# Kernel tuning notes

Hardware: AMD Instinct MI355X
Metric: run time of the kernel (lower is better)

## Reference

```python
import jax, jax.numpy as jnp
import numpy as np

N_NODES = 50000
N_EDGES = 800000
DIMS = [128, 512, 256, 128]
EPS = 1e-5


def setup_inputs() -> dict:
    key = jax.random.key(0)
    ks = jax.random.split(key, 2 + 5 * 3)
    inp = {
        "x": jax.random.normal(ks[0], (N_NODES, DIMS[0]), dtype=jnp.float32),
        "edge_index": jax.random.randint(ks[1], (2, N_EDGES), 0, N_NODES, dtype=jnp.int64),
    }
    ki = 2
    for i in range(3):
        din, dout = DIMS[i], DIMS[i + 1]
        s = 1.0 / np.sqrt(din)
        inp[f"Wl{i}"] = jax.random.uniform(ks[ki + 0], (din, dout), jnp.float32, -s, s)
        inp[f"bl{i}"] = jax.random.uniform(ks[ki + 1], (dout,), jnp.float32, -s, s)
        inp[f"Wr{i}"] = jax.random.uniform(ks[ki + 2], (din, dout), jnp.float32, -s, s)
        inp[f"g{i}"] = jnp.ones((dout,), jnp.float32)
        inp[f"b{i}"] = jnp.zeros((dout,), jnp.float32)
        ki += 5
    return inp


def _sage_mean(x, src, dst, Wl, bl, Wr):
    n = x.shape[0]
    agg = jax.ops.segment_sum(x[src], dst, num_segments=n)  # [N, din]
    deg = jax.ops.segment_sum(jnp.ones((src.shape[0],), x.dtype), dst, num_segments=n)
    mean = agg / jnp.maximum(deg, 1.0)[:, None]
    return mean @ Wl + bl + x @ Wr


def _bn(h, gamma, beta):
    m = h.mean(axis=0)
    v = h.var(axis=0)
    return gamma * (h - m) * jax.lax.rsqrt(v + EPS) + beta


def reference(x, edge_index, Wl0, bl0, Wr0, g0, b0, Wl1, bl1, Wr1, g1, b1, Wl2, bl2, Wr2, g2, b2):
    src, dst = edge_index[0], edge_index[1]
    params = [(Wl0, bl0, Wr0, g0, b0), (Wl1, bl1, Wr1, g1, b1), (Wl2, bl2, Wr2, g2, b2)]
    h = x
    for Wl, bl, Wr, g, b in params:
        h = _sage_mean(h, src, dst, Wl, bl, Wr)
        h = _bn(h, g, b)
        h = jax.nn.relu(h)
        # dropout: identity in eval mode
    return h
```

## Files before the change

kernel.cpp:

```cpp
#include <hip/hip_runtime.h>
#include <cstdint>
#include <cstddef>


#define EPS_BN 1e-5f

typedef unsigned short ushort_t;
typedef __attribute__((ext_vector_type(8))) short short8;
typedef __attribute__((ext_vector_type(4))) float float4v;
typedef __attribute__((ext_vector_type(2))) float float2v;
typedef __attribute__((ext_vector_type(2))) unsigned int uint2v;
typedef __attribute__((ext_vector_type(4))) unsigned int uint4v;

__device__ __forceinline__ float bflo(unsigned int w) {
    union { unsigned int i; float f; } v; v.i = w << 16; return v.f;
}
__device__ __forceinline__ float bfhi(unsigned int w) {
    union { unsigned int i; float f; } v; v.i = w & 0xffff0000u; return v.f;
}
__device__ __forceinline__ ushort_t f2bf(float f) {
    union { float f; unsigned int i; } v; v.f = f;
    unsigned int r = v.i + 0x7fffu + ((v.i >> 16) & 1u);
    return (ushort_t)(r >> 16);
}

__device__ __forceinline__ void async_copy16(void* lds, const void* g) {
    __builtin_amdgcn_global_load_lds(
        (const __attribute__((address_space(1))) unsigned int*)g,
        (__attribute__((address_space(3))) unsigned int*)lds, 16, 0, 0);
}

__device__ __forceinline__ void edge_sd(const int* __restrict__ p, int e, int ne,
                                        bool is64, int& s, int& d) {
    if (is64) { s = p[2 * e];  d = p[2 * ne + 2 * e]; }
    else      { s = p[e];      d = p[ne + e]; }
}
__device__ __forceinline__ int edge_d(const int* __restrict__ p, int e, int ne, bool is64) {
    return is64 ? p[2 * ne + 2 * e] : p[ne + e];
}

__device__ __forceinline__ bool detect_is64(const int* __restrict__ edges,
                                            int* sh_flag, int t) {
    if (t == 0) *sh_flag = 1;
    __syncthreads();
    if (t < 64 && edges[2 * t + 1] != 0) *sh_flag = 0;
    __syncthreads();
    return *sh_flag != 0;
}

#define EPB 2048

__global__ __launch_bounds__(256) void bhist_kernel(
    const int* __restrict__ edges, int ne, int* __restrict__ gcnt) {
    __shared__ int h[256];
    __shared__ int f64;
    int t = threadIdx.x;
    bool is64 = detect_is64(edges, &f64, t);
    h[t] = 0;
    __syncthreads();
    int base_e = blockIdx.x * EPB;
    #pragma unroll
    for (int u = 0; u < EPB / 256; ++u) {
        int i = base_e + u * 256 + t;
        if (i < ne) atomicAdd(&h[edge_d(edges, i, ne, is64) >> 8], 1);
    }
    __syncthreads();
    if (h[t]) atomicAdd(&gcnt[t], h[t]);
}

__global__ __launch_bounds__(256) void bscan_kernel(
    const int* __restrict__ gcnt, int nb, int ne,
    int* __restrict__ bbase, int* __restrict__ bcur) {
    __shared__ int sh[256];
    int t = threadIdx.x;
    int v = (t < nb) ? gcnt[t] : 0;
    sh[t] = v;
    __syncthreads();
    for (int o = 1; o < 256; o <<= 1) {
        int x = (t >= o) ? sh[t - o] : 0;
        __syncthreads();
        sh[t] += x;
        __syncthreads();
    }
    int excl = sh[t] - v;
    if (t < nb) { bbase[t] = excl; bcur[t] = excl; }
    if (t == nb) bbase[t] = ne;
    if (t == 0 && nb == 256) bbase[256] = ne;
}

__global__ __launch_bounds__(256) void bscatter_kernel(
    const int* __restrict__ edges, int ne,
    int* __restrict__ bcur, int* __restrict__ packed) {
    __shared__ int h[256];
    __shared__ int chunkb[256];
    __shared__ int lcur[256];
    __shared__ int f64;
    int t = threadIdx.x;
    bool is64 = detect_is64(edges, &f64, t);
    h[t] = 0;
    lcur[t] = 0;
    __syncthreads();
    int base_e = blockIdx.x * EPB;
    int ent[EPB / 256], eb[EPB / 256];
    #pragma unroll
    for (int u = 0; u < EPB / 256; ++u) {
        int i = base_e + u * 256 + t;
        if (i < ne) {
            int s, d;
            edge_sd(edges, i, ne, is64, s, d);
            ent[u] = s | ((d & 255) << 24);
            eb[u] = d >> 8;
            atomicAdd(&h[eb[u]], 1);
        } else eb[u] = -1;
    }
    __syncthreads();
    if (h[t]) chunkb[t] = atomicAdd(&bcur[t], h[t]);
    __syncthreads();
    #pragma unroll
    for (int u = 0; u < EPB / 256; ++u) {
        if (eb[u] >= 0) {
            int lp = atomicAdd(&lcur[eb[u]], 1);
            packed[chunkb[eb[u]] + lp] = ent[u];
        }
    }
}

__global__ __launch_bounds__(256) void bbuild_kernel(
    const int* __restrict__ packed, const int* __restrict__ bbase,
    int* __restrict__ rowptr, int* __restrict__ csr_src, int n) {
    __shared__ int h[256];
    __shared__ int cur[256];
    int t = threadIdx.x;
    int bb = blockIdx.x;
    int base = bbase[bb], cnt = bbase[bb + 1] - base;
    h[t] = 0;
    __syncthreads();
    for (int i = t; i < cnt; i += 256)
        atomicAdd(&h[(unsigned)packed[base + i] >> 24], 1);
    __syncthreads();
    int v = h[t];
    for (int o = 1; o < 256; o <<= 1) {
        int x = (t >= o) ? h[t - o] : 0;
        __syncthreads();
        h[t] += x;
        __syncthreads();
    }
    int excl = h[t] - v;
    int node = bb * 256 + t;
    if (node <= n) rowptr[node] = base + excl;
    cur[t] = excl;
    __syncthreads();
    for (int i = t; i < cnt; i += 256) {
        int e = packed[base + i];
        int lp = atomicAdd(&cur[(unsigned)e >> 24], 1);
        csr_src[base + lp] = e & 0xffffff;
    }
}

__global__ void prep_all_kernel(
    const float* __restrict__ x, ushort_t* __restrict__ xb, int nxb,
    const float* __restrict__ Wl0, const float* __restrict__ Wr0,
    ushort_t* __restrict__ WT0, int nb0,
    const float* __restrict__ Wl1, const float* __restrict__ Wr1,
    ushort_t* __restrict__ WT1c, int nb1,
    const float* __restrict__ Wl2, const float* __restrict__ Wr2,
    ushort_t* __restrict__ WT2c) {
    const int D0 = 128, D1 = 512, D2 = 256, D3 = 128;
    int b = blockIdx.x;
    if (b < nxb) {
        int i = b * 256 + threadIdx.x;
        xb[i] = f2bf(x[i]);
        return;
    }
    b -= nxb;
    if (b < nb0) {
        int idx = b * 256 + threadIdx.x;
        int K2 = 2 * D0;
        int nn = idx / K2, k = idx - nn * K2;
        float v = (k < D0) ? Wl0[(size_t)k * D1 + nn] : Wr0[(size_t)(k - D0) * D1 + nn];
        WT0[idx] = f2bf(v);
        return;
    }
    b -= nb0;
    if (b < nb1) {
        int idx = b * 256 + threadIdx.x;
        int nn = idx / D1, k = idx - nn * D1;
        float v = (nn < D2) ? Wl1[(size_t)k * D2 + nn] : Wr1[(size_t)k * D2 + (nn - D2)];
        WT1c[idx] = f2bf(v);
        return;
    }
    b -= nb1;
    {
        int idx = b * 256 + threadIdx.x;
        int nn = idx / D2, k = idx - nn * D2;
        float v = (nn < D3) ? Wl2[(size_t)k * D3 + nn] : Wr2[(size_t)k * D3 + (nn - D3)];
        WT2c[idx] = f2bf(v);
    }
}

template <int VEC> struct VecT;
template <> struct VecT<2> { using T = unsigned int; };
template <> struct VecT<4> { using T = uint2v; };
template <> struct VecT<8> { using T = uint4v; };

template <int VEC>
__device__ __forceinline__ void vunpack(typename VecT<VEC>::T v, unsigned int* w) {
    if constexpr (VEC == 2) { w[0] = v; }
    else if constexpr (VEC == 4) { w[0] = v.x; w[1] = v.y; }
    else { w[0] = v.x; w[1] = v.y; w[2] = v.z; w[3] = v.w; }
}

template <int VEC>
__device__ __forceinline__ void vaccum(typename VecT<VEC>::T v, float* acc) {
    unsigned int w[VEC / 2];
    vunpack<VEC>(v, w);
    #pragma unroll
    for (int i = 0; i < VEC / 2; ++i) {
        acc[2 * i + 0] += bflo(w[i]);
        acc[2 * i + 1] += bfhi(w[i]);
    }
}

template <int VEC>
__device__ __forceinline__ void gather_sum(
    const ushort_t* __restrict__ base, const int* __restrict__ csr_src,
    int e0, int e1, int rstride, float* acc) {
    using VT = typename VecT<VEC>::T;
    int e = e0;
    for (; e + 16 <= e1; e += 16) {
        VT v[16];
        #pragma unroll
        for (int u = 0; u < 16; ++u)
            v[u] = *(const VT*)(base + (size_t)csr_src[e + u] * rstride);
        #pragma unroll
        for (int u = 0; u < 16; ++u) vaccum<VEC>(v[u], acc);
    }
    if (e + 8 <= e1) {
        VT v[8];
        #pragma unroll
        for (int u = 0; u < 8; ++u)
            v[u] = *(const VT*)(base + (size_t)csr_src[e + u] * rstride);
        #pragma unroll
        for (int u = 0; u < 8; ++u) vaccum<VEC>(v[u], acc);
        e += 8;
    }
    if (e + 4 <= e1) {
        VT v[4];
        #pragma unroll
        for (int u = 0; u < 4; ++u)
            v[u] = *(const VT*)(base + (size_t)csr_src[e + u] * rstride);
        #pragma unroll
        for (int u = 0; u < 4; ++u) vaccum<VEC>(v[u], acc);
        e += 4;
    }
    if (e + 2 <= e1) {
        VT v0 = *(const VT*)(base + (size_t)csr_src[e] * rstride);
        VT v1 = *(const VT*)(base + (size_t)csr_src[e + 1] * rstride);
        vaccum<VEC>(v0, acc); vaccum<VEC>(v1, acc);
        e += 2;
    }
    if (e < e1)
        vaccum<VEC>(*(const VT*)(base + (size_t)csr_src[e] * rstride), acc);
}

template <int VEC>
__global__ __launch_bounds__(256) void aggregate_wave_kernel(
    const ushort_t* __restrict__ h, ushort_t* __restrict__ mean,
    const int* __restrict__ rowptr, const int* __restrict__ csr_src, int nnodes) {
    const int din = VEC * 64;
    const int wave = threadIdx.x >> 6;
    const int lane = threadIdx.x & 63;
    const int wstride = gridDim.x * 4;
    using VT = typename VecT<VEC>::T;
    for (int wid = blockIdx.x * 4 + wave; wid < nnodes; wid += wstride) {
        int e0 = rowptr[wid], e1 = rowptr[wid + 1];
        float acc[VEC];
        #pragma unroll
        for (int i = 0; i < VEC; ++i) acc[i] = 0.f;
        gather_sum<VEC>(h + (size_t)lane * VEC, csr_src, e0, e1, din, acc);

        int deg = e1 - e0;
        float scale = 1.0f / (float)(deg > 1 ? deg : 1);
        unsigned int o[VEC / 2];
        #pragma unroll
        for (int i = 0; i < VEC / 2; ++i)
            o[i] = (unsigned int)f2bf(acc[2 * i] * scale) |
                   ((unsigned int)f2bf(acc[2 * i + 1] * scale) << 16);
        VT ov;
        if constexpr (VEC == 2) { ov = o[0]; }
        else if constexpr (VEC == 4) { ov.x = o[0]; ov.y = o[1]; }
        else { ov.x = o[0]; ov.y = o[1]; ov.z = o[2]; ov.w = o[3]; }
        *(VT*)(mean + (size_t)wid * din + (size_t)lane * VEC) = ov;
    }
}

template <int VEC>
__global__ __launch_bounds__(256) void aggregate_add_kernel(
    const ushort_t* __restrict__ PR, const float* __restrict__ bias,
    ushort_t* __restrict__ pre,
    const int* __restrict__ rowptr, const int* __restrict__ csr_src, int nnodes,
    float* __restrict__ gsum, float* __restrict__ gsq) {
    const int D = VEC * 64;
    const int stride = 2 * D;
    __shared__ float s_red[2][4][VEC * 64];
    const int wave = threadIdx.x >> 6;
    const int lane = threadIdx.x & 63;
    const int wstride = gridDim.x * 4;
    using VT = typename VecT<VEC>::T;

    float ssum[VEC], ssq[VEC];
    #pragma unroll
    for (int i = 0; i < VEC; ++i) { ssum[i] = 0.f; ssq[i] = 0.f; }

    for (int wid = blockIdx.x * 4 + wave; wid < nnodes; wid += wstride) {
        int e0 = rowptr[wid], e1 = rowptr[wid + 1];
        float acc[VEC];
        #pragma unroll
        for (int i = 0; i < VEC; ++i) acc[i] = 0.f;
        gather_sum<VEC>(PR + (size_t)lane * VEC, csr_src, e0, e1, stride, acc);

        int deg = e1 - e0;
        float scale = 1.0f / (float)(deg > 1 ? deg : 1);

        VT rv = *(const VT*)(PR + (size_t)wid * stride + D + (size_t)lane * VEC);
        unsigned int rw[VEC / 2];
        vunpack<VEC>(rv, rw);
        float o[VEC];
        #pragma unroll
        for (int i = 0; i < VEC / 2; ++i) {
            o[2 * i + 0] = bflo(rw[i]);
            o[2 * i + 1] = bfhi(rw[i]);
        }
        #pragma unroll
        for (int i = 0; i < VEC; ++i) {
            o[i] += acc[i] * scale + bias[lane * VEC + i];
            ssum[i] += o[i];
            ssq[i] += o[i] * o[i];
        }

        unsigned int ow[VEC / 2];
        #pragma unroll
        for (int i = 0; i < VEC / 2; ++i)
            ow[i] = (unsigned int)f2bf(o[2 * i]) | ((unsigned int)f2bf(o[2 * i + 1]) << 16);
        VT ov;
        if constexpr (VEC == 2) { ov = ow[0]; }
        else if constexpr (VEC == 4) { ov.x = ow[0]; ov.y = ow[1]; }
        else { ov.x = ow[0]; ov.y = ow[1]; ov.z = ow[2]; ov.w = ow[3]; }
        *(VT*)(pre + (size_t)wid * D + (size_t)lane * VEC) = ov;
    }

    #pragma unroll
    for (int i = 0; i < VEC; ++i) {
        s_red[0][wave][lane * VEC + i] = ssum[i];
        s_red[1][wave][lane * VEC + i] = ssq[i];
    }
    __syncthreads();
    int t = threadIdx.x;
    if (t < D) {
        float a = s_red[0][0][t] + s_red[0][1][t] + s_red[0][2][t] + s_red[0][3][t];
        float q = s_red[1][0][t] + s_red[1][1][t] + s_red[1][2][t] + s_red[1][3][t];
        atomicAdd(&gsum[t], a);
        atomicAdd(&gsq[t], q);
    }
}

template <bool DUAL, bool BIAS, bool STATS>
__global__ __launch_bounds__(512) void gemm_glds_kernel(
    const ushort_t* __restrict__ A1, const ushort_t* __restrict__ A2,
    const ushort_t* __restrict__ BT, const float* __restrict__ bias,
    ushort_t* __restrict__ Cb, int N, int K1, int Ktot, int Wtot,
    float* __restrict__ gsum, float* __restrict__ gsq) {
    __shared__ ushort_t As[2 * 256 * 32];
    __shared__ ushort_t Bs[2 * 128 * 32];

    const int tid = threadIdx.x;
    const int wave = tid >> 6;
    const int lane = tid & 63;
    const int quad = lane >> 4;
    const int l15 = lane & 15;
    const int sw3 = l15 & 3;
    const int rowBase = blockIdx.y * 256;
    const int colBase = blockIdx.x * 128;
    const int wm = (wave >> 1) * 64;
    const int wn = (wave & 1) * 64;

    float4v acc[4][4];
    #pragma unroll
    for (int i = 0; i < 4; ++i)
        #pragma unroll
        for (int j = 0; j < 4; ++j)
            acc[i][j] = (float4v){0.f, 0.f, 0.f, 0.f};

    const int nkt = Ktot / 32;
    const int khalf = K1 / 32;

    auto stage = [&](int buf, int kt) {
        const ushort_t* Asrc = A1;
        int kg = kt * 32;
        if (DUAL && kt >= khalf) { Asrc = A2; kg = (kt - khalf) * 32; }
        const int kb = kt * 32;
        #pragma unroll
        for (int u = 0; u < 2; ++u) {
            int c = u * 512 + tid;
            int r = c >> 2, cc = c & 3;
            int off = (cc ^ (r & 3)) * 8;
            int grow = rowBase + r;
            if (grow >= N) grow = N - 1;
            async_copy16(&As[buf * 8192 + c * 8], Asrc + (size_t)grow * K1 + kg + off);
        }
        {
            int c = tid;
            int r = c >> 2, cc = c & 3;
            int off = (cc ^ (r & 3)) * 8;
            async_copy16(&Bs[buf * 4096 + c * 8], BT + (size_t)(colBase + r) * Ktot + kb + off);
        }
    };

    stage(0, 0);
    int cur = 0;
    for (int kt = 0; kt < nkt; ++kt) {
        if (kt + 1 < nkt) {
            stage(cur ^ 1, kt + 1);
            asm volatile("s_waitcnt vmcnt(3)\n\ts_barrier" ::: "memory");
        } else {
            asm volatile("s_waitcnt vmcnt(0)\n\ts_barrier" ::: "memory");
        }

        short8 af[4], bf4[4];
        #pragma unroll
        for (int i = 0; i < 4; ++i)
            af[i] = *(const short8*)&As[cur * 8192 + (wm + i * 16 + l15) * 32 + (quad ^ sw3) * 8];
        #pragma unroll
        for (int j = 0; j < 4; ++j)
            bf4[j] = *(const short8*)&Bs[cur * 4096 + (wn + j * 16 + l15) * 32 + (quad ^ sw3) * 8];
        __builtin_amdgcn_s_setprio(1);
        #pragma unroll
        for (int i = 0; i < 4; ++i)
            #pragma unroll
            for (int j = 0; j < 4; ++j)
                acc[i][j] = __builtin_amdgcn_mfma_f32_16x16x32_bf16(bf4[j], af[i], acc[i][j], 0, 0, 0);
        __builtin_amdgcn_s_setprio(0);
        asm volatile("s_barrier" ::: "memory");
        cur ^= 1;
    }

    float cs[4][4], cq[4][4];
    if constexpr (STATS) {
        #pragma unroll
        for (int j = 0; j < 4; ++j)
            #pragma unroll
            for (int r = 0; r < 4; ++r) { cs[j][r] = 0.f; cq[j][r] = 0.f; }
    }

    ushort_t* lws = &As[wave * 2048];
    #pragma unroll
    for (int p = 0; p < 2; ++p) {
        #pragma unroll
        for (int jj = 0; jj < 2; ++jj) {
            int j = 2 * p + jj;
            float4 bv = make_float4(0.f, 0.f, 0.f, 0.f);
            if (BIAS) bv = *(const float4*)(bias + colBase + wn + j * 16 + quad * 4);
            #pragma unroll
            for (int i = 0; i < 4; ++i) {
                float v0 = acc[i][j][0] + bv.x;
                float v1 = acc[i][j][1] + bv.y;
                float v2 = acc[i][j][2] + bv.z;
                float v3 = acc[i][j][3] + bv.w;
                if constexpr (STATS) {
                    if (rowBase + wm + i * 16 + l15 < N) {
                        cs[j][0] += v0; cq[j][0] += v0 * v0;
                        cs[j][1] += v1; cq[j][1] += v1 * v1;
                        cs[j][2] += v2; cq[j][2] += v2 * v2;
                        cs[j][3] += v3; cq[j][3] += v3 * v3;
                    }
                }
                uint2 pk;
                pk.x = (unsigned int)f2bf(v0) | ((unsigned int)f2bf(v1) << 16);
                pk.y = (unsigned int)f2bf(v2) | ((unsigned int)f2bf(v3) << 16);
                *(uint2*)&lws[(i * 16 + l15) * 32 + jj * 16 + quad * 4] = pk;
            }
        }
        __syncthreads();
        #pragma unroll
        for (int it = 0; it < 4; ++it) {
            int c = it * 64 + lane;
            int row = c >> 2, coff = (c & 3) * 8;
            int grow = rowBase + wm + row;
            if (grow < N) {
                uint4 v = *(const uint4*)&lws[row * 32 + coff];
                *(uint4*)(Cb + (size_t)grow * Wtot + colBase + wn + p * 32 + coff) = v;
            }
        }
        __syncthreads();
    }

    if constexpr (STATS) {
        #pragma unroll
        for (int j = 0; j < 4; ++j)
            #pragma unroll
            for (int r = 0; r < 4; ++r) {
                #pragma unroll
                for (int m = 1; m < 16; m <<= 1) {
                    cs[j][r] += __shfl_xor(cs[j][r], m);
                    cq[j][r] += __shfl_xor(cq[j][r], m);
                }
            }
        if (l15 == 0) {
            #pragma unroll
            for (int j = 0; j < 4; ++j)
                #pragma unroll
                for (int r = 0; r < 4; ++r) {
                    int col = colBase + wn + j * 16 + quad * 4 + r;
                    atomicAdd(&gsum[col], cs[j][r]);
                    atomicAdd(&gsq[col], cq[j][r]);
                }
        }
    }
}

__global__ void bn_relu_b2b_kernel(const ushort_t* __restrict__ h, ushort_t* __restrict__ hb,
                                   int N, int D,
                                   const float* __restrict__ sum, const float* __restrict__ sumsq,
                                   const float* __restrict__ g, const float* __restrict__ b) {
    size_t idx = (size_t)blockIdx.x * blockDim.x + threadIdx.x;
    size_t tot = (size_t)N * D / 2;
    if (idx >= tot) return;
    int cp = (int)(idx & (size_t)(D / 2 - 1));
    int c0 = cp * 2, c1 = c0 + 1;
    float m0 = sum[c0] / (float)N, m1 = sum[c1] / (float)N;
    float i0 = rsqrtf(sumsq[c0] / (float)N - m0 * m0 + EPS_BN);
    float i1 = rsqrtf(sumsq[c1] / (float)N - m1 * m1 + EPS_BN);
    unsigned int w = ((const unsigned int*)h)[idx];
    float v0 = g[c0] * (bflo(w) - m0) * i0 + b[c0];
    float v1 = g[c1] * (bfhi(w) - m1) * i1 + b[c1];
    v0 = v0 > 0.f ? v0 : 0.f;
    v1 = v1 > 0.f ? v1 : 0.f;
    ((unsigned int*)hb)[idx] = (unsigned int)f2bf(v0) | ((unsigned int)f2bf(v1) << 16);
}

__global__ void bn_relu_b2f_kernel(const ushort_t* __restrict__ h, float* __restrict__ hf,
                                   int N, int D,
                                   const float* __restrict__ sum, const float* __restrict__ sumsq,
                                   const float* __restrict__ g, const float* __restrict__ b) {
    size_t idx = (size_t)blockIdx.x * blockDim.x + threadIdx.x;
    size_t tot = (size_t)N * D / 2;
    if (idx >= tot) return;
    int cp = (int)(idx & (size_t)(D / 2 - 1));
    int c0 = cp * 2, c1 = c0 + 1;
    float m0 = sum[c0] / (float)N, m1 = sum[c1] / (float)N;
    float i0 = rsqrtf(sumsq[c0] / (float)N - m0 * m0 + EPS_BN);
    float i1 = rsqrtf(sumsq[c1] / (float)N - m1 * m1 + EPS_BN);
    unsigned int w = ((const unsigned int*)h)[idx];
    float v0 = g[c0] * (bflo(w) - m0) * i0 + b[c0];
    float v1 = g[c1] * (bfhi(w) - m1) * i1 + b[c1];
    float2v o;
    o.x = v0 > 0.f ? v0 : 0.f;
    o.y = v1 > 0.f ? v1 : 0.f;
    *(float2v*)(hf + idx * 2) = o;
}

extern "C" void kernel_launch(void* const* d_in, const int* in_sizes, int n_in,
                              void* d_out, int out_size, void* d_ws, size_t ws_size,
                              hipStream_t stream) {
    const float* x     = (const float*)d_in[0];
    const int*   edges = (const int*)d_in[1];
    const float* Wl0 = (const float*)d_in[2];
    const float* bl0 = (const float*)d_in[3];
    const float* Wr0 = (const float*)d_in[4];
    const float* g0  = (const float*)d_in[5];
    const float* b0  = (const float*)d_in[6];
    const float* Wl1 = (const float*)d_in[7];
    const float* bl1 = (const float*)d_in[8];
    const float* Wr1 = (const float*)d_in[9];
    const float* g1  = (const float*)d_in[10];
    const float* b1  = (const float*)d_in[11];
    const float* Wl2 = (const float*)d_in[12];
    const float* bl2 = (const float*)d_in[13];
    const float* Wr2 = (const float*)d_in[14];
    const float* g2  = (const float*)d_in[15];
    const float* b2  = (const float*)d_in[16];

    const int D0 = 128, D1 = 512, D2 = 256, D3 = 128;
    const int n  = in_sizes[0] / D0;
    const int ne = in_sizes[1] / 2;
    const int NB = (n + 255) >> 8;

    char* base = (char*)d_ws;
    size_t off = 0;
    auto alloc = [&](size_t bytes) -> char* {
        char* p = base + off;
        off = (off + bytes + 255) & ~(size_t)255;
        return p;
    };
    int*      gcnt    = (int*)alloc(256 * 4);
    float*    stats   = (float*)alloc(6 * 512 * 4);
    size_t    zero_span = off;
    int*      bbase   = (int*)alloc(257 * 4);
    int*      bcur    = (int*)alloc(256 * 4);
    int*      packed  = (int*)alloc((size_t)ne * 4);
    int*      rowptr  = (int*)alloc((size_t)(n + 1) * 4);
    int*      csr_src = (int*)alloc((size_t)ne * 4);
    ushort_t* xb      = (ushort_t*)alloc((size_t)n * D0 * 2);
    ushort_t* mb      = (ushort_t*)alloc((size_t)n * 512 * 2);
    ushort_t* h1b     = (ushort_t*)alloc((size_t)n * D1 * 2);
    ushort_t* h2b     = (ushort_t*)alloc((size_t)n * D2 * 2);
    ushort_t* hpre    = (ushort_t*)alloc((size_t)n * 512 * 2);
    ushort_t* WT0     = (ushort_t*)alloc((size_t)D1 * 2 * D0 * 2);
    ushort_t* WT1c    = (ushort_t*)alloc((size_t)(2 * D2) * D1 * 2);
    ushort_t* WT2c    = (ushort_t*)alloc((size_t)(2 * D3) * D2 * 2);
    float*    out     = (float*)d_out;
    (void)ws_size; (void)n_in; (void)out_size;

    hipMemsetAsync(base, 0, zero_span, stream);

    int ablk = (ne + EPB - 1) / EPB;
    bhist_kernel<<<ablk, 256, 0, stream>>>(edges, ne, gcnt);
    bscan_kernel<<<1, 256, 0, stream>>>(gcnt, NB, ne, bbase, bcur);
    bscatter_kernel<<<ablk, 256, 0, stream>>>(edges, ne, bcur, packed);
    bbuild_kernel<<<NB, 256, 0, stream>>>(packed, bbase, rowptr, csr_src, n);

    const int nxb = (n * D0) / 256;
    const int nb0 = (D1 * 2 * D0) / 256;
    const int nb1 = (2 * D2 * D1) / 256;
    const int nb2 = (2 * D3 * D2) / 256;
    prep_all_kernel<<<nxb + nb0 + nb1 + nb2, 256, 0, stream>>>(
        x, xb, nxb, Wl0, Wr0, WT0, nb0, Wl1, Wr1, WT1c, nb1, Wl2, Wr2, WT2c);

    const int aggGrid = 2048;
    const int rowBlocks = (n + 255) / 256;
    float* st0 = stats + 0 * 1024;
    float* st1 = stats + 1 * 1024;
    float* st2 = stats + 2 * 1024;

    aggregate_wave_kernel<2><<<aggGrid, 256, 0, stream>>>(xb, mb, rowptr, csr_src, n);
    gemm_glds_kernel<true, true, true><<<dim3(D1 / 128, rowBlocks), 512, 0, stream>>>(
        mb, xb, WT0, bl0, hpre, n, D0, 2 * D0, D1, st0, st0 + 512);
    bn_relu_b2b_kernel<<<((size_t)n * D1 / 2 + 255) / 256, 256, 0, stream>>>(
        hpre, h1b, n, D1, st0, st0 + 512, g0, b0);

    gemm_glds_kernel<false, false, false><<<dim3(2 * D2 / 128, rowBlocks), 512, 0, stream>>>(
        h1b, nullptr, WT1c, nullptr, mb, n, D1, D1, 2 * D2, nullptr, nullptr);
    aggregate_add_kernel<4><<<aggGrid, 256, 0, stream>>>(
        mb, bl1, hpre, rowptr, csr_src, n, st1, st1 + 512);
    bn_relu_b2b_kernel<<<((size_t)n * D2 / 2 + 255) / 256, 256, 0, stream>>>(
        hpre, h2b, n, D2, st1, st1 + 512, g1, b1);

    gemm_glds_kernel<false, false, false><<<dim3(2 * D3 / 128, rowBlocks), 512, 0, stream>>>(
        h2b, nullptr, WT2c, nullptr, mb, n, D2, D2, 2 * D3, nullptr, nullptr);
    aggregate_add_kernel<2><<<aggGrid, 256, 0, stream>>>(
        mb, bl2, hpre, rowptr, csr_src, n, st2, st2 + 512);
    bn_relu_b2f_kernel<<<((size_t)n * D3 / 2 + 255) / 256, 256, 0, stream>>>(
        hpre, out, n, D3, st2, st2 + 512, g2, b2);
}
```

Before: 607.0 us.

## Shrink GEMM tile to 128x128 with 256 threads and XCD-aware block remap

The GEMM workgroup tile shrinks from 256x128 with 512 threads to 128x128 with 256 threads. Launch bounds now request 4 blocks per CU, and the shared-memory footprint and staging loops are adjusted to match. A 1D grid is remapped so that consecutive logical tiles land on the same XCD, which aims for better L2 reuse of the A and B tiles across chiplets. The intent is better occupancy and tile-to-cache locality. In exchange, each output element gets less data reuse from the tile, and twice as many blocks reload B.

```diff
diff --git a/kernel.cpp b/kernel.cpp
--- a/kernel.cpp
+++ b/kernel.cpp
@@ -365,12 +365,12 @@
 }
 
 template <bool DUAL, bool BIAS, bool STATS>
-__global__ __launch_bounds__(512) void gemm_glds_kernel(
+__global__ __launch_bounds__(256, 4) void gemm_glds_kernel(
     const ushort_t* __restrict__ A1, const ushort_t* __restrict__ A2,
     const ushort_t* __restrict__ BT, const float* __restrict__ bias,
-    ushort_t* __restrict__ Cb, int N, int K1, int Ktot, int Wtot,
+    ushort_t* __restrict__ Cb, int N, int K1, int Ktot, int Wtot, int nxShift,
     float* __restrict__ gsum, float* __restrict__ gsq) {
-    __shared__ ushort_t As[2 * 256 * 32];
+    __shared__ ushort_t As[2 * 128 * 32];
     __shared__ ushort_t Bs[2 * 128 * 32];
 
     const int tid = threadIdx.x;
@@ -379,8 +379,17 @@
     const int quad = lane >> 4;
     const int l15 = lane & 15;
     const int sw3 = l15 & 3;
-    const int rowBase = blockIdx.y * 256;
-    const int colBase = blockIdx.x * 128;
+
+    const int nwg = gridDim.x;
+    const int q = nwg >> 3, rr = nwg & 7;
+    const int o = blockIdx.x;
+    const int xcd = o & 7, sub = o >> 3;
+    const int wgid = (xcd < rr ? xcd * (q + 1) : rr * (q + 1) + (xcd - rr) * q) + sub;
+    const int bx = wgid & ((1 << nxShift) - 1);
+    const int by = wgid >> nxShift;
+
+    const int rowBase = by * 128;
+    const int colBase = bx * 128;
     const int wm = (wave >> 1) * 64;
     const int wn = (wave & 1) * 64;
 
@@ -401,15 +410,16 @@
         const int kb = kt * 32;
         #pragma unroll
         for (int u = 0; u < 2; ++u) {
-            int c = u * 512 + tid;
+            int c = u * 256 + tid;
             int r = c >> 2, cc = c & 3;
             int off = (cc ^ (r & 3)) * 8;
             int grow = rowBase + r;
             if (grow >= N) grow = N - 1;
-            async_copy16(&As[buf * 8192 + c * 8], Asrc + (size_t)grow * K1 + kg + off);
-        }
-        {
-            int c = tid;
+            async_copy16(&As[buf * 4096 + c * 8], Asrc + (size_t)grow * K1 + kg + off);
+        }
+        #pragma unroll
+        for (int u = 0; u < 2; ++u) {
+            int c = u * 256 + tid;
             int r = c >> 2, cc = c & 3;
             int off = (cc ^ (r & 3)) * 8;
             async_copy16(&Bs[buf * 4096 + c * 8], BT + (size_t)(colBase + r) * Ktot + kb + off);
@@ -421,7 +431,7 @@
     for (int kt = 0; kt < nkt; ++kt) {
         if (kt + 1 < nkt) {
             stage(cur ^ 1, kt + 1);
-            asm volatile("s_waitcnt vmcnt(3)\n\ts_barrier" ::: "memory");
+            asm volatile("s_waitcnt vmcnt(4)\n\ts_barrier" ::: "memory");
         } else {
             asm volatile("s_waitcnt vmcnt(0)\n\ts_barrier" ::: "memory");
         }
@@ -429,7 +439,7 @@
         short8 af[4], bf4[4];
         #pragma unroll
         for (int i = 0; i < 4; ++i)
-            af[i] = *(const short8*)&As[cur * 8192 + (wm + i * 16 + l15) * 32 + (quad ^ sw3) * 8];
+            af[i] = *(const short8*)&As[cur * 4096 + (wm + i * 16 + l15) * 32 + (quad ^ sw3) * 8];
         #pragma unroll
         for (int j = 0; j < 4; ++j)
             bf4[j] = *(const short8*)&Bs[cur * 4096 + (wn + j * 16 + l15) * 32 + (quad ^ sw3) * 8];
@@ -627,26 +637,26 @@
         x, xb, nxb, Wl0, Wr0, WT0, nb0, Wl1, Wr1, WT1c, nb1, Wl2, Wr2, WT2c);
 
     const int aggGrid = 2048;
-    const int rowBlocks = (n + 255) / 256;
+    const int rowBlocks = (n + 127) / 128;
     float* st0 = stats + 0 * 1024;
     float* st1 = stats + 1 * 1024;
     float* st2 = stats + 2 * 1024;
 
     aggregate_wave_kernel<2><<<aggGrid, 256, 0, stream>>>(xb, mb, rowptr, csr_src, n);
-    gemm_glds_kernel<true, true, true><<<dim3(D1 / 128, rowBlocks), 512, 0, stream>>>(
-        mb, xb, WT0, bl0, hpre, n, D0, 2 * D0, D1, st0, st0 + 512);
+    gemm_glds_kernel<true, true, true><<<4 * rowBlocks, 256, 0, stream>>>(
+        mb, xb, WT0, bl0, hpre, n, D0, 2 * D0, D1, 2, st0, st0 + 512);
     bn_relu_b2b_kernel<<<((size_t)n * D1 / 2 + 255) / 256, 256, 0, stream>>>(
         hpre, h1b, n, D1, st0, st0 + 512, g0, b0);
 
-    gemm_glds_kernel<false, false, false><<<dim3(2 * D2 / 128, rowBlocks), 512, 0, stream>>>(
-        h1b, nullptr, WT1c, nullptr, mb, n, D1, D1, 2 * D2, nullptr, nullptr);
+    gemm_glds_kernel<false, false, false><<<4 * rowBlocks, 256, 0, stream>>>(
+        h1b, nullptr, WT1c, nullptr, mb, n, D1, D1, 2 * D2, 2, nullptr, nullptr);
     aggregate_add_kernel<4><<<aggGrid, 256, 0, stream>>>(
         mb, bl1, hpre, rowptr, csr_src, n, st1, st1 + 512);
     bn_relu_b2b_kernel<<<((size_t)n * D2 / 2 + 255) / 256, 256, 0, stream>>>(
         hpre, h2b, n, D2, st1, st1 + 512, g1, b1);
 
-    gemm_glds_kernel<false, false, false><<<dim3(2 * D3 / 128, rowBlocks), 512, 0, stream>>>(
-        h2b, nullptr, WT2c, nullptr, mb, n, D2, D2, 2 * D3, nullptr, nullptr);
+    gemm_glds_kernel<false, false, false><<<2 * rowBlocks, 256, 0, stream>>>(
+        h2b, nullptr, WT2c, nullptr, mb, n, D2, D2, 2 * D3, 1, nullptr, nullptr);
     aggregate_add_kernel<2><<<aggGrid, 256, 0, stream>>>(
         mb, bl2, hpre, rowptr, csr_src, n, st2, st2 + 512);
     bn_relu_b2f_kernel<<<((size_t)n * D3 / 2 + 255) / 256, 256, 0, stream>>>(
```

Result: faster. 570.9 us, median of 2 (-5.9%).
